# Kernel optimization log

Hardware: AMD Instinct MI355X
Metric: run time of the kernel (lower is better)

Reference implementation:

```python
import jax, jax.numpy as jnp
import numpy as np
import math

B, S, D, H, DH, DFF = 2, 2048, 2048, 16, 128, 8192
EPS = 1e-6
K_AMB = -1.0


def log_map_origin(x, K):
    # x: (..., d+1) Lorentz point -> tangent vector (..., d)
    xi = x[..., 1:]
    n = jnp.sqrt(jnp.sum(xi * xi, axis=-1, keepdims=True))
    a = jnp.sqrt(-K) * n
    # asinh(a)/a, stable near 0 (on-manifold, acosh(sqrt(-K)x0) == asinh(sqrt(-K)||xi||))
    f = jnp.where(a < 1e-6, 1.0 - a * a / 6.0, jnp.arcsinh(a) / jnp.maximum(a, 1e-12))
    return f * xi


def exp_map_stable(v, K):
    # v: (..., d) tangent -> Lorentz point (..., d+1); x0 from exact constraint
    n = jnp.sqrt(jnp.sum(v * v, axis=-1, keepdims=True))
    a = jnp.sqrt(-K) * n
    sinc = jnp.where(a < 1e-6, 1.0 + a * a / 6.0, jnp.sinh(a) / jnp.maximum(a, 1e-12))
    xi = sinc * v
    x0 = jnp.sqrt(-1.0 / K + jnp.sum(xi * xi, axis=-1, keepdims=True))
    return jnp.concatenate([x0, xi], axis=-1)


def lorentz_rmsnorm(x, scale):
    v = log_map_origin(x, K_AMB)
    rms = jnp.sqrt(jnp.mean(v * v, axis=-1, keepdims=True) + EPS)
    return exp_map_stable(scale * (v / rms), K_AMB)


def per_head_attention(x_normed, mask, Wq, Wk, Wv, Wo, head_K):
    v = log_map_origin(x_normed, K_AMB)  # (B,S,D)
    def split(w):
        return (v @ w).reshape(B, S, H, DH).transpose(0, 2, 1, 3)  # (B,H,S,DH)
    q, k, vv = split(Wq), split(Wk), split(Wv)
    Kh = head_K[None, :, None, None]  # (1,H,1,1) per-head curvature
    ql = exp_map_stable(q, Kh)  # (B,H,S,DH+1)
    kl = exp_map_stable(k, Kh)
    # Lorentz inner product <q,k>_L = -q0 k0 + qi.ki via signed metric
    metric = jnp.concatenate([-jnp.ones((1,)), jnp.ones((DH,))])
    L = jnp.einsum('bhqd,bhkd->bhqk', ql * metric, kl)
    # negative squared-distance proxy: 2<q,k>_L - 2/K  (zero when q==k)
    scores = (2.0 * L - 2.0 / Kh) / math.sqrt(DH)
    scores = jnp.where(mask[None, None, :, :], scores, -1e30)
    attn = jax.nn.softmax(scores, axis=-1)
    out = jnp.einsum('bhqk,bhkd->bhqd', attn, vv)  # (B,H,S,DH)
    out = out.transpose(0, 2, 1, 3).reshape(B, S, H * DH)
    return out @ Wo  # Euclidean (B,S,D)


def block_forward(x, mask, scale1, scale2, Wq, Wk, Wv, Wo, head_K, W1, W2):
    xn = lorentz_rmsnorm(x, scale1)
    attn_out = per_head_attention(xn, mask, Wq, Wk, Wv, Wo, head_K)
    x = exp_map_stable(log_map_origin(x, K_AMB) + attn_out, K_AMB)
    xn = lorentz_rmsnorm(x, scale2)
    vf = log_map_origin(xn, K_AMB)
    ffn_eu_pre = jax.nn.gelu(vf @ W1, approximate=False) @ W2
    ffn_out = exp_map_stable(ffn_eu_pre, K_AMB)
    x = exp_map_stable(log_map_origin(x, K_AMB) + log_map_origin(ffn_out, K_AMB), K_AMB)
    return x


def setup_inputs() -> dict:
    key = jax.random.key(0)
    ks = jax.random.split(key, 9)
    v0 = jax.random.normal(ks[0], (B, S, D), jnp.float32) * 0.02
    x = exp_map_stable(v0, K_AMB)  # on-manifold input (B,S,D+1)
    mask = jnp.tril(jnp.ones((S, S), bool))  # causal: True = attend
    init_scale = 1.0 / math.sqrt(D)
    w_std = 0.02
    return {
        'x': x,
        'mask': mask,
        'scale1': jnp.full((D,), init_scale, jnp.float32),
        'scale2': jnp.full((D,), init_scale, jnp.float32),
        'Wq': jax.random.normal(ks[1], (D, H * DH), jnp.float32) * w_std,
        'Wk': jax.random.normal(ks[2], (D, H * DH), jnp.float32) * w_std,
        'Wv': jax.random.normal(ks[3], (D, H * DH), jnp.float32) * w_std,
        'Wo': jax.random.normal(ks[4], (H * DH, D), jnp.float32) * w_std,
        'head_K': jnp.full((H,), -1.0, jnp.float32),
        'W1': jax.random.normal(ks[5], (D, DFF), jnp.float32) * w_std,
        'W2': jax.random.normal(ks[6], (DFF, D), jnp.float32) * w_std,
    }


def reference(x, mask, scale1, scale2, Wq, Wk, Wv, Wo, head_K, W1, W2):
    return block_forward(x, mask, scale1, scale2, Wq, Wk, Wv, Wo, head_K, W1, W2)
```

## Files before the change

kernel.cpp:

```cpp
#include <hip/hip_runtime.h>
#include <stdint.h>

typedef unsigned short u16;
typedef __attribute__((ext_vector_type(8))) short bf16x8;
typedef __attribute__((ext_vector_type(4))) float f32x4;

#define SEQ    2048
#define NB     2
#define NHEAD  16
#define DHEAD  128
#define DMODEL 2048
#define DFFN   8192
#define MROWS  4096

__device__ __forceinline__ u16 f2bf(float x) {
  union { float f; uint32_t u; } v; v.f = x;
  return (u16)((v.u + 0x7fffu + ((v.u >> 16) & 1u)) >> 16);
}
__device__ __forceinline__ float bf2f(u16 h) {
  union { uint32_t u; float f; } v; v.u = ((uint32_t)h) << 16;
  return v.f;
}
__device__ __forceinline__ void gload16(const void* g, void* l) {
  __builtin_amdgcn_global_load_lds((const __attribute__((address_space(1))) void*)g,
                                   (__attribute__((address_space(3))) void*)l,
                                   16, 0, 0);
}
__device__ __forceinline__ float blockSum256(float v) {
  __shared__ float red[4];
  #pragma unroll
  for (int m = 1; m < 64; m <<= 1) v += __shfl_xor(v, m, 64);
  int w = threadIdx.x >> 6;
  if ((threadIdx.x & 63) == 0) red[w] = v;
  __syncthreads();
  float s = red[0] + red[1] + red[2] + red[3];
  __syncthreads();
  return s;
}

__global__ void transpose_w(const float* __restrict__ in, u16* __restrict__ out, int R, int C) {
  __shared__ float tile[32][33];
  int c0 = blockIdx.x * 32, r0 = blockIdx.y * 32;
  int tx = threadIdx.x, ty = threadIdx.y;
  #pragma unroll
  for (int i = 0; i < 4; ++i)
    tile[ty + 8*i][tx] = in[(size_t)(r0 + ty + 8*i) * C + c0 + tx];
  __syncthreads();
  #pragma unroll
  for (int i = 0; i < 4; ++i)
    out[(size_t)(c0 + ty + 8*i) * R + r0 + tx] = f2bf(tile[tx][ty + 8*i]);
}

__global__ void ln_first(const float* __restrict__ x, const float* __restrict__ scale,
                         float* __restrict__ v1, u16* __restrict__ t1) {
  int row = blockIdx.x;
  const float* xr = x + (size_t)row * (DMODEL + 1) + 1;
  float vals[8]; float ss = 0.f;
  #pragma unroll
  for (int i = 0; i < 8; ++i) {
    int idx = threadIdx.x + 256 * i;
    vals[i] = xr[idx];
    ss += vals[i] * vals[i];
  }
  ss = blockSum256(ss);
  float n = sqrtf(ss);
  float f = (n < 1e-6f) ? (1.0f - n * n * (1.0f/6.0f)) : (asinhf(n) / n);
  float rms = sqrtf(f * f * ss * (1.0f / DMODEL) + 1e-6f);
  float ir = 1.0f / rms;
  #pragma unroll
  for (int i = 0; i < 8; ++i) {
    int idx = threadIdx.x + 256 * i;
    float v = f * vals[i];
    v1[(size_t)row * DMODEL + idx] = v;
    t1[(size_t)row * DMODEL + idx] = f2bf(scale[idx] * v * ir);
  }
}

__global__ void rms_mid(const float* __restrict__ u, const float* __restrict__ scale,
                        u16* __restrict__ t) {
  int row = blockIdx.x;
  const float* ur = u + (size_t)row * DMODEL;
  float vals[8]; float ss = 0.f;
  #pragma unroll
  for (int i = 0; i < 8; ++i) { int idx = threadIdx.x + 256*i; vals[i] = ur[idx]; ss += vals[i]*vals[i]; }
  ss = blockSum256(ss);
  float ir = 1.0f / sqrtf(ss * (1.0f / DMODEL) + 1e-6f);
  #pragma unroll
  for (int i = 0; i < 8; ++i) {
    int idx = threadIdx.x + 256*i;
    t[(size_t)row*DMODEL + idx] = f2bf(scale[idx]*vals[i]*ir);
  }
}

__global__ void final_exp(const float* __restrict__ u, float* __restrict__ out) {
  int row = blockIdx.x;
  const float* ur = u + (size_t)row * DMODEL;
  float vals[8]; float ss = 0.f;
  #pragma unroll
  for (int i = 0; i < 8; ++i) { int idx = threadIdx.x + 256*i; vals[i] = ur[idx]; ss += vals[i]*vals[i]; }
  ss = blockSum256(ss);
  float n = sqrtf(ss);
  float f = (n < 1e-6f) ? (1.0f + n*n*(1.0f/6.0f)) : (sinhf(n)/n);
  float* orow = out + (size_t)row * (DMODEL + 1);
  if (threadIdx.x == 0) orow[0] = sqrtf(1.0f + f*f*ss);
  #pragma unroll
  for (int i = 0; i < 8; ++i) { int idx = threadIdx.x + 256*i; orow[1+idx] = f*vals[i]; }
}

template<int EPI>
__global__ __launch_bounds__(256, 3) void gemm_bt(
    const u16* __restrict__ A, const u16* __restrict__ Bt,
    u16* __restrict__ Cb, float* Cf, const float* add,
    int M, int N, int K)
{
  __shared__ u16 As[128 * 32];
  __shared__ u16 Bs[128 * 32];
  const int tid = threadIdx.x;
  const int w = tid >> 6, lane = tid & 63;
  const int lrow = lane & 15, kq = lane >> 4;
  const int m0 = blockIdx.y * 128, n0 = blockIdx.x * 128;
  const int wm = w >> 1, wn = w & 1;
  f32x4 acc[4][4] = {};
  for (int k0 = 0; k0 < K; k0 += 32) {
    __syncthreads();
    #pragma unroll
    for (int j = 0; j < 2; ++j) {
      int ebase = j * 2048 + w * 512;
      int e = ebase + lane * 8;
      int row = e >> 5, col = e & 31;
      gload16(A  + (size_t)(m0 + row) * K + k0 + col, &As[ebase]);
      gload16(Bt + (size_t)(n0 + row) * K + k0 + col, &Bs[ebase]);
    }
    __syncthreads();
    bf16x8 av[4], bv[4];
    #pragma unroll
    for (int i = 0; i < 4; ++i) av[i] = *(const bf16x8*)&As[(wm*64 + i*16 + lrow)*32 + kq*8];
    #pragma unroll
    for (int j = 0; j < 4; ++j) bv[j] = *(const bf16x8*)&Bs[(wn*64 + j*16 + lrow)*32 + kq*8];
    #pragma unroll
    for (int i = 0; i < 4; ++i)
      #pragma unroll
      for (int j = 0; j < 4; ++j)
        acc[i][j] = __builtin_amdgcn_mfma_f32_16x16x32_bf16(av[i], bv[j], acc[i][j], 0, 0, 0);
  }
  #pragma unroll
  for (int i = 0; i < 4; ++i)
    #pragma unroll
    for (int j = 0; j < 4; ++j)
      #pragma unroll
      for (int r = 0; r < 4; ++r) {
        int row = m0 + wm*64 + i*16 + kq*4 + r;
        int col = n0 + wn*64 + j*16 + lrow;
        size_t idx = (size_t)row * N + col;
        float v = acc[i][j][r];
        if (EPI == 0) {
          Cb[idx] = f2bf(v);
        } else if (EPI == 1) {
          Cf[idx] = v + add[idx];
        } else {
          float g = 0.5f * v * (1.0f + erff(v * 0.70710678118654752f));
          Cb[idx] = f2bf(g);
        }
      }
}

__global__ void prep_qk(const u16* __restrict__ in, const float* __restrict__ headK,
                        u16* __restrict__ Lout, float* __restrict__ l0,
                        int instride, int off) {
  int gid = blockIdx.x * 4 + (threadIdx.x >> 6);
  int lane = threadIdx.x & 63;
  int b = gid >> 15;
  int rem = gid & 32767;
  int h = rem >> 11;
  int s = rem & 2047;
  const u16* src = in + ((size_t)(b * SEQ + s)) * instride + off + h * DHEAD + lane * 2;
  float v0 = bf2f(src[0]), v1 = bf2f(src[1]);
  float nn = v0*v0 + v1*v1;
  #pragma unroll
  for (int m = 1; m < 64; m <<= 1) nn += __shfl_xor(nn, m, 64);
  float Kh = headK[h];
  float sk = sqrtf(-Kh);
  float a = sk * sqrtf(nn);
  float f = (a < 1e-6f) ? (1.0f + a*a*(1.0f/6.0f)) : (sinhf(a) / a);
  u16* dst = Lout + (size_t)gid * DHEAD + lane * 2;
  dst[0] = f2bf(f * v0);
  dst[1] = f2bf(f * v1);
  if (lane == 0) l0[gid] = sqrtf(-1.0f/Kh + f*f*nn);
}

__global__ void vtrans(const u16* __restrict__ vb, u16* __restrict__ VT,
                       int instride, int off) {
  __shared__ u16 tile[32][33];
  int bh = blockIdx.x;
  int b = bh >> 4, h = bh & 15;
  int s0 = blockIdx.y * 32, d0 = blockIdx.z * 32;
  int tx = threadIdx.x, ty = threadIdx.y;
  #pragma unroll
  for (int i = 0; i < 4; ++i)
    tile[ty + 8*i][tx] = vb[((size_t)(b*SEQ + s0 + ty + 8*i)) * instride + off + h*DHEAD + d0 + tx];
  __syncthreads();
  #pragma unroll
  for (int i = 0; i < 4; ++i)
    VT[((size_t)bh*DHEAD + d0 + ty + 8*i) * SEQ + s0 + tx] = tile[tx][ty + 8*i];
}

__global__ __launch_bounds__(256, 2) void attn_kernel(
    const u16* __restrict__ Ql, const u16* __restrict__ Kl,
    const u16* __restrict__ VT, const float* __restrict__ ql0,
    const float* __restrict__ kl0, const float* __restrict__ headK,
    u16* __restrict__ out) {
  __shared__ u16 klds[2][32 * 128];
  __shared__ u16 vlds[2][128 * 32];
  __shared__ u16 plds[4][32 * 36];
  const int tid = threadIdx.x, w = tid >> 6, lane = tid & 63;
  const int lrow = lane & 15, kq = lane >> 4;
  const int id = blockIdx.x;
  const int bh = id & 31;
  const int qb = 15 - (id >> 5);
  const int q0 = qb * 128 + w * 32;
  const int b = bh >> 4, h = bh & 15;
  const float Kh = headK[h];
  const float LOG2E = 1.44269504088896f;
  const float isd = 0.088388347648318447f;
  const float sc_mul = 2.0f * isd * LOG2E;
  const float sc_add = (-2.0f / Kh) * isd * LOG2E;

  const u16* kbase  = Kl + (size_t)bh * SEQ * DHEAD;
  const u16* vtbase = VT + (size_t)bh * DHEAD * SEQ;
  const float* kl0b = kl0 + (size_t)bh * SEQ;
  u16* pw = &plds[w][0];

  bf16x8 aq[2][4];
  const u16* qbase = Ql + ((size_t)bh * SEQ + q0) * DHEAD;
  #pragma unroll
  for (int m = 0; m < 2; ++m)
    #pragma unroll
    for (int dc = 0; dc < 4; ++dc)
      aq[m][dc] = *(const bf16x8*)&qbase[(size_t)(m*16 + lrow) * DHEAD + dc*32 + kq*8];
  float q0r[2][4];
  #pragma unroll
  for (int m = 0; m < 2; ++m)
    #pragma unroll
    for (int r = 0; r < 4; ++r)
      q0r[m][r] = ql0[(size_t)bh * SEQ + q0 + m*16 + kq*4 + r];

  auto stage = [&](int k0, int buf) {
    #pragma unroll
    for (int i = 0; i < 2; ++i) {
      int rl = w*8 + i*4 + (lane >> 4);
      int c = (lane & 15) ^ (rl & 15);
      gload16(kbase + ((size_t)(k0 + rl)) * DHEAD + c * 8,
              &klds[buf][(w*8 + i*4) * 128]);
    }
    #pragma unroll
    for (int i = 0; i < 2; ++i) {
      int rl = w*32 + i*16 + (lane >> 2);
      int c = (lane & 3) ^ ((rl >> 1) & 3);
      gload16(vtbase + (size_t)rl * SEQ + k0 + c * 8,
              &vlds[buf][(w*32 + i*16) * 32]);
    }
  };

  float lacc[2][4] = {};
  f32x4 o[2][8] = {};
  const int niter = qb * 4 + 4;

  stage(0, 0);
  for (int i = 0; i < niter; ++i) {
    const int k0 = i * 32, buf = i & 1;
    float kc0 = kl0b[k0 + lrow];
    float kc1 = kl0b[k0 + 16 + lrow];
    if (i + 1 < niter) {
      stage(k0 + 32, buf ^ 1);
      asm volatile("s_waitcnt vmcnt(4)" ::: "memory");
    } else {
      asm volatile("s_waitcnt vmcnt(0)" ::: "memory");
    }
    asm volatile("s_barrier" ::: "memory");

    f32x4 sc[2][2] = {};
    #pragma unroll
    for (int dc = 0; dc < 4; ++dc) {
      int c = dc*4 + kq;
      bf16x8 bk0 = *(const bf16x8*)&klds[buf][lrow*128        + (c ^ (lrow & 15)) * 8];
      bf16x8 bk1 = *(const bf16x8*)&klds[buf][(16 + lrow)*128 + (c ^ ((16 + lrow) & 15)) * 8];
      #pragma unroll
      for (int m = 0; m < 2; ++m) {
        sc[m][0] = __builtin_amdgcn_mfma_f32_16x16x32_bf16(aq[m][dc], bk0, sc[m][0], 0, 0, 0);
        sc[m][1] = __builtin_amdgcn_mfma_f32_16x16x32_bf16(aq[m][dc], bk1, sc[m][1], 0, 0, 0);
      }
    }
    #pragma unroll
    for (int m = 0; m < 2; ++m)
      #pragma unroll
      for (int r = 0; r < 4; ++r) {
        int qg = q0 + m*16 + kq*4 + r;
        float p0 = exp2f((sc[m][0][r] - q0r[m][r] * kc0) * sc_mul + sc_add);
        float p1 = exp2f((sc[m][1][r] - q0r[m][r] * kc1) * sc_mul + sc_add);
        p0 = (k0 + lrow      <= qg) ? p0 : 0.f;
        p1 = (k0 + 16 + lrow <= qg) ? p1 : 0.f;
        lacc[m][r] += p0 + p1;
        pw[(m*16 + kq*4 + r) * 36 + lrow]      = f2bf(p0);
        pw[(m*16 + kq*4 + r) * 36 + 16 + lrow] = f2bf(p1);
      }
    bf16x8 ap0 = *(const bf16x8*)&pw[(size_t)lrow * 36 + kq*8];
    bf16x8 ap1 = *(const bf16x8*)&pw[(size_t)(16 + lrow) * 36 + kq*8];
    int vc = (kq ^ ((lrow >> 1) & 3)) * 8;
    #pragma unroll
    for (int n = 0; n < 8; ++n) {
      bf16x8 bv = *(const bf16x8*)&vlds[buf][(n*16 + lrow) * 32 + vc];
      o[0][n] = __builtin_amdgcn_mfma_f32_16x16x32_bf16(ap0, bv, o[0][n], 0, 0, 0);
      o[1][n] = __builtin_amdgcn_mfma_f32_16x16x32_bf16(ap1, bv, o[1][n], 0, 0, 0);
    }
    asm volatile("s_barrier" ::: "memory");
  }

  float rcl[2][4];
  #pragma unroll
  for (int m = 0; m < 2; ++m)
    #pragma unroll
    for (int r = 0; r < 4; ++r) {
      float s = lacc[m][r];
      #pragma unroll
      for (int mm = 1; mm < 16; mm <<= 1) s += __shfl_xor(s, mm, 16);
      rcl[m][r] = 1.0f / s;
    }
  #pragma unroll
  for (int m = 0; m < 2; ++m)
    #pragma unroll
    for (int n = 0; n < 8; ++n)
      #pragma unroll
      for (int r = 0; r < 4; ++r) {
        int qg = q0 + m*16 + kq*4 + r;
        out[((size_t)b * SEQ + qg) * DMODEL + h * DHEAD + n*16 + lrow] =
            f2bf(o[m][n][r] * rcl[m][r]);
      }
}

extern "C" void kernel_launch(void* const* d_in, const int* in_sizes, int n_in,
                              void* d_out, int out_size, void* d_ws, size_t ws_size,
                              hipStream_t stream) {
  const float* x      = (const float*)d_in[0];
  const float* scale1 = (const float*)d_in[2];
  const float* scale2 = (const float*)d_in[3];
  const float* Wq     = (const float*)d_in[4];
  const float* Wk     = (const float*)d_in[5];
  const float* Wv     = (const float*)d_in[6];
  const float* Wo     = (const float*)d_in[7];
  const float* headK  = (const float*)d_in[8];
  const float* W1     = (const float*)d_in[9];
  const float* W2     = (const float*)d_in[10];
  float* out = (float*)d_out;

  char* p = (char*)d_ws;
  size_t off = 0;
  auto take = [&](size_t bytes) -> char* {
    char* r = p + off;
    off += (bytes + 255) & ~(size_t)255;
    return r;
  };
  u16* WqT = (u16*)take((size_t)DMODEL*DMODEL*2);
  u16* WkT = (u16*)take((size_t)DMODEL*DMODEL*2);
  u16* WvT = (u16*)take((size_t)DMODEL*DMODEL*2);
  u16* WoT = (u16*)take((size_t)DMODEL*DMODEL*2);
  u16* W1T = (u16*)take((size_t)DMODEL*DFFN*2);
  u16* W2T = (u16*)take((size_t)DMODEL*DFFN*2);
  float* vres = (float*)take((size_t)MROWS*DMODEL*4);
  u16* tbuf = (u16*)take((size_t)MROWS*DMODEL*2);
  u16* qkvb = (u16*)take((size_t)MROWS*3*DMODEL*2);
  u16* Qlb  = (u16*)take((size_t)MROWS*DMODEL*2);
  u16* Klb  = (u16*)take((size_t)MROWS*DMODEL*2);
  u16* VTb  = (u16*)take((size_t)MROWS*DMODEL*2);
  float* q0b = (float*)take((size_t)NB*NHEAD*SEQ*4);
  float* k0b = (float*)take((size_t)NB*NHEAD*SEQ*4);
  u16* hbuf = qkvb;
  u16* attnout = tbuf;

  dim3 tb(32, 8);
  transpose_w<<<dim3(DMODEL/32, DMODEL/32), tb, 0, stream>>>(Wq, WqT, DMODEL, DMODEL);
  transpose_w<<<dim3(DMODEL/32, DMODEL/32), tb, 0, stream>>>(Wk, WkT, DMODEL, DMODEL);
  transpose_w<<<dim3(DMODEL/32, DMODEL/32), tb, 0, stream>>>(Wv, WvT, DMODEL, DMODEL);
  transpose_w<<<dim3(DMODEL/32, DMODEL/32), tb, 0, stream>>>(Wo, WoT, DMODEL, DMODEL);
  transpose_w<<<dim3(DFFN/32,   DMODEL/32), tb, 0, stream>>>(W1, W1T, DMODEL, DFFN);
  transpose_w<<<dim3(DMODEL/32, DFFN/32),   tb, 0, stream>>>(W2, W2T, DFFN, DMODEL);

  ln_first<<<MROWS, 256, 0, stream>>>(x, scale1, vres, tbuf);

  gemm_bt<0><<<dim3(3*DMODEL/128, MROWS/128), 256, 0, stream>>>(tbuf, WqT, qkvb, nullptr, nullptr, MROWS, 3*DMODEL, DMODEL);

  prep_qk<<<NB*NHEAD*SEQ/4, 256, 0, stream>>>(qkvb, headK, Qlb, q0b, 3*DMODEL, 0);
  prep_qk<<<NB*NHEAD*SEQ/4, 256, 0, stream>>>(qkvb, headK, Klb, k0b, 3*DMODEL, DMODEL);
  vtrans<<<dim3(NB*NHEAD, SEQ/32, DHEAD/32), tb, 0, stream>>>(qkvb, VTb, 3*DMODEL, 2*DMODEL);

  attn_kernel<<<dim3(512), 256, 0, stream>>>(Qlb, Klb, VTb, q0b, k0b, headK, attnout);

  gemm_bt<1><<<dim3(DMODEL/128, MROWS/128), 256, 0, stream>>>(attnout, WoT, nullptr, vres, vres, MROWS, DMODEL, DMODEL);

  rms_mid<<<MROWS, 256, 0, stream>>>(vres, scale2, tbuf);

  gemm_bt<2><<<dim3(DFFN/128, MROWS/128), 256, 0, stream>>>(tbuf, W1T, hbuf, nullptr, nullptr, MROWS, DFFN, DMODEL);

  gemm_bt<1><<<dim3(DMODEL/128, MROWS/128), 256, 0, stream>>>(hbuf, W2T, nullptr, vres, vres, MROWS, DMODEL, DFFN);

  final_exp<<<MROWS, 256, 0, stream>>>(vres, out);

  (void)in_sizes; (void)n_in; (void)out_size; (void)ws_size;
}
```

Before: 1.015 ms.

## Replace GEMM with 256x256 tiled, double-buffered, swizzled-LDS 512-thread kernel

Replaces the 128x128 single-buffered GEMM with a 256x256 tile kernel using 8 waves, 64-wide K steps, and double-buffered LDS with prefetch of the next tiles interleaved between MFMA phases. It adds an XOR swizzle on LDS addresses to avoid bank conflicts, s_setprio around MFMA bursts, and a block-ID remap for L2 locality across XCDs. The aim is to hide global-load latency and raise MFMA utilization in all four GEMMs. In exchange it uses 128KB of LDS per block and hand-placed waitcnt/barriers, which is fragile, and the grid for the N=2048 GEMMs is small at 128 blocks.

```diff
diff --git a/kernel.cpp b/kernel.cpp
--- a/kernel.cpp
+++ b/kernel.cpp
@@ -108,48 +108,147 @@
 }
 
 template<int EPI>
-__global__ __launch_bounds__(256, 3) void gemm_bt(
+__global__ __launch_bounds__(512, 2) void gemm256(
     const u16* __restrict__ A, const u16* __restrict__ Bt,
     u16* __restrict__ Cb, float* Cf, const float* add,
     int M, int N, int K)
 {
-  __shared__ u16 As[128 * 32];
-  __shared__ u16 Bs[128 * 32];
+  __shared__ __attribute__((aligned(128))) char smem[131072];
   const int tid = threadIdx.x;
   const int w = tid >> 6, lane = tid & 63;
   const int lrow = lane & 15, kq = lane >> 4;
-  const int m0 = blockIdx.y * 128, n0 = blockIdx.x * 128;
-  const int wm = w >> 1, wn = w & 1;
-  f32x4 acc[4][4] = {};
-  for (int k0 = 0; k0 < K; k0 += 32) {
-    __syncthreads();
-    #pragma unroll
-    for (int j = 0; j < 2; ++j) {
-      int ebase = j * 2048 + w * 512;
-      int e = ebase + lane * 8;
-      int row = e >> 5, col = e & 31;
-      gload16(A  + (size_t)(m0 + row) * K + k0 + col, &As[ebase]);
-      gload16(Bt + (size_t)(n0 + row) * K + k0 + col, &Bs[ebase]);
-    }
-    __syncthreads();
-    bf16x8 av[4], bv[4];
-    #pragma unroll
-    for (int i = 0; i < 4; ++i) av[i] = *(const bf16x8*)&As[(wm*64 + i*16 + lrow)*32 + kq*8];
-    #pragma unroll
-    for (int j = 0; j < 4; ++j) bv[j] = *(const bf16x8*)&Bs[(wn*64 + j*16 + lrow)*32 + kq*8];
+  const int wm = w >> 2, wn = w & 3;
+
+  const int nwg = gridDim.x;
+  const int cpx = nwg >> 3;
+  const int sid = (blockIdx.x & 7) * cpx + (blockIdx.x >> 3);
+  const int NX = N >> 8;
+  const int bx = sid % NX, by = sid / NX;
+  const int m0 = by * 256, n0 = bx * 256;
+  const int NT = K >> 6;
+
+  size_t goff[2];
+  #pragma unroll
+  for (int r = 0; r < 2; ++r) {
+    int L = r * 8192 + tid * 16;
+    int U = L ^ (((L >> 9) & 1) << 5);
+    int si = U >> 10;
+    int row = (si >> 1) * 16 + ((U >> 6) & 15);
+    int col = (si & 1) * 32 + ((U & 63) >> 1);
+    goff[r] = (size_t)row * K + col;
+  }
+  auto stage_half = [&](const u16* g, int ldsOff) {
+    #pragma unroll
+    for (int r = 0; r < 2; ++r)
+      gload16(g + goff[r], smem + ldsOff + r * 8192 + w * 1024);
+  };
+
+  const u16* A0 = A  + (size_t)m0 * K;
+  const u16* A1 = A  + (size_t)(m0 + 128) * K;
+  const u16* B0 = Bt + (size_t)n0 * K;
+  const u16* B1 = Bt + (size_t)(n0 + 128) * K;
+
+  const int aoff = (lrow * 64 + kq * 16) ^ ((lrow & 8) << 2);
+
+  f32x4 acc[8][4] = {};
+
+  stage_half(A0, 0);
+  stage_half(A1, 16384);
+  stage_half(B0, 32768);
+  stage_half(B1, 49152);
+  stage_half(A0 + 64, 65536);
+  stage_half(A1 + 64, 65536 + 16384);
+  asm volatile("s_waitcnt vmcnt(4)" ::: "memory");
+  asm volatile("s_barrier" ::: "memory");
+
+  for (int t = 0; t < NT; ++t) {
+    const int buf = t & 1;
+    const char* ab = smem + buf * 65536 + wm * 16384 + aoff;
+    const char* bb = smem + buf * 65536 + 32768 + (wn >> 1) * 16384 + (wn & 1) * 8192 + aoff;
+    bf16x8 a0[4][2], a1[4][2], b0[2][2], b1[2][2];
+
     #pragma unroll
     for (int i = 0; i < 4; ++i)
       #pragma unroll
-      for (int j = 0; j < 4; ++j)
-        acc[i][j] = __builtin_amdgcn_mfma_f32_16x16x32_bf16(av[i], bv[j], acc[i][j], 0, 0, 0);
+      for (int kk = 0; kk < 2; ++kk)
+        a0[i][kk] = *(const bf16x8*)(ab + (i*2 + kk) * 1024);
+    #pragma unroll
+    for (int j = 0; j < 2; ++j)
+      #pragma unroll
+      for (int kk = 0; kk < 2; ++kk)
+        b0[j][kk] = *(const bf16x8*)(bb + (j*2 + kk) * 1024);
+    if (t + 1 < NT) stage_half(B0 + (t+1)*64, (buf^1)*65536 + 32768);
+    asm volatile("s_barrier" ::: "memory");
+    __builtin_amdgcn_s_setprio(1);
+    #pragma unroll
+    for (int kk = 0; kk < 2; ++kk)
+      #pragma unroll
+      for (int i = 0; i < 4; ++i)
+        #pragma unroll
+        for (int j = 0; j < 2; ++j)
+          acc[i][j] = __builtin_amdgcn_mfma_f32_16x16x32_bf16(a0[i][kk], b0[j][kk], acc[i][j], 0, 0, 0);
+    __builtin_amdgcn_s_setprio(0);
+    asm volatile("s_barrier" ::: "memory");
+
+    #pragma unroll
+    for (int i = 0; i < 4; ++i)
+      #pragma unroll
+      for (int kk = 0; kk < 2; ++kk)
+        a1[i][kk] = *(const bf16x8*)(ab + ((4 + i)*2 + kk) * 1024);
+    if (t + 1 < NT) stage_half(B1 + (t+1)*64, (buf^1)*65536 + 49152);
+    asm volatile("s_barrier" ::: "memory");
+    __builtin_amdgcn_s_setprio(1);
+    #pragma unroll
+    for (int kk = 0; kk < 2; ++kk)
+      #pragma unroll
+      for (int i = 0; i < 4; ++i)
+        #pragma unroll
+        for (int j = 0; j < 2; ++j)
+          acc[4 + i][j] = __builtin_amdgcn_mfma_f32_16x16x32_bf16(a1[i][kk], b0[j][kk], acc[4 + i][j], 0, 0, 0);
+    __builtin_amdgcn_s_setprio(0);
+    asm volatile("s_barrier" ::: "memory");
+
+    #pragma unroll
+    for (int j = 0; j < 2; ++j)
+      #pragma unroll
+      for (int kk = 0; kk < 2; ++kk)
+        b1[j][kk] = *(const bf16x8*)(bb + ((2 + j)*2 + kk) * 1024);
+    if (t + 2 < NT) stage_half(A0 + (t+2)*64, buf*65536);
+    asm volatile("s_barrier" ::: "memory");
+    __builtin_amdgcn_s_setprio(1);
+    #pragma unroll
+    for (int kk = 0; kk < 2; ++kk)
+      #pragma unroll
+      for (int i = 0; i < 4; ++i)
+        #pragma unroll
+        for (int j = 0; j < 2; ++j)
+          acc[4 + i][2 + j] = __builtin_amdgcn_mfma_f32_16x16x32_bf16(a1[i][kk], b1[j][kk], acc[4 + i][2 + j], 0, 0, 0);
+    __builtin_amdgcn_s_setprio(0);
+    asm volatile("s_barrier" ::: "memory");
+
+    if (t + 2 < NT) stage_half(A1 + (t+2)*64, buf*65536 + 16384);
+    asm volatile("s_barrier" ::: "memory");
+    __builtin_amdgcn_s_setprio(1);
+    #pragma unroll
+    for (int kk = 0; kk < 2; ++kk)
+      #pragma unroll
+      for (int i = 0; i < 4; ++i)
+        #pragma unroll
+        for (int j = 0; j < 2; ++j)
+          acc[i][2 + j] = __builtin_amdgcn_mfma_f32_16x16x32_bf16(a0[i][kk], b1[j][kk], acc[i][2 + j], 0, 0, 0);
+    __builtin_amdgcn_s_setprio(0);
+    if (t + 2 < NT) asm volatile("s_waitcnt vmcnt(4)" ::: "memory");
+    else            asm volatile("s_waitcnt vmcnt(0)" ::: "memory");
+    asm volatile("s_barrier" ::: "memory");
   }
-  #pragma unroll
-  for (int i = 0; i < 4; ++i)
+
+  #pragma unroll
+  for (int i = 0; i < 8; ++i)
     #pragma unroll
     for (int j = 0; j < 4; ++j)
       #pragma unroll
       for (int r = 0; r < 4; ++r) {
-        int row = m0 + wm*64 + i*16 + kq*4 + r;
+        int row = m0 + wm*128 + i*16 + kq*4 + r;
         int col = n0 + wn*64 + j*16 + lrow;
         size_t idx = (size_t)row * N + col;
         float v = acc[i][j][r];
@@ -386,7 +485,8 @@
 
   ln_first<<<MROWS, 256, 0, stream>>>(x, scale1, vres, tbuf);
 
-  gemm_bt<0><<<dim3(3*DMODEL/128, MROWS/128), 256, 0, stream>>>(tbuf, WqT, qkvb, nullptr, nullptr, MROWS, 3*DMODEL, DMODEL);
+  gemm256<0><<<dim3((3*DMODEL/256)*(MROWS/256)), 512, 0, stream>>>(
+      tbuf, WqT, qkvb, nullptr, nullptr, MROWS, 3*DMODEL, DMODEL);
 
   prep_qk<<<NB*NHEAD*SEQ/4, 256, 0, stream>>>(qkvb, headK, Qlb, q0b, 3*DMODEL, 0);
   prep_qk<<<NB*NHEAD*SEQ/4, 256, 0, stream>>>(qkvb, headK, Klb, k0b, 3*DMODEL, DMODEL);
@@ -394,13 +494,16 @@
 
   attn_kernel<<<dim3(512), 256, 0, stream>>>(Qlb, Klb, VTb, q0b, k0b, headK, attnout);
 
-  gemm_bt<1><<<dim3(DMODEL/128, MROWS/128), 256, 0, stream>>>(attnout, WoT, nullptr, vres, vres, MROWS, DMODEL, DMODEL);
+  gemm256<1><<<dim3((DMODEL/256)*(MROWS/256)), 512, 0, stream>>>(
+      attnout, WoT, nullptr, vres, vres, MROWS, DMODEL, DMODEL);
 
   rms_mid<<<MROWS, 256, 0, stream>>>(vres, scale2, tbuf);
 
-  gemm_bt<2><<<dim3(DFFN/128, MROWS/128), 256, 0, stream>>>(tbuf, W1T, hbuf, nullptr, nullptr, MROWS, DFFN, DMODEL);
-
-  gemm_bt<1><<<dim3(DMODEL/128, MROWS/128), 256, 0, stream>>>(hbuf, W2T, nullptr, vres, vres, MROWS, DMODEL, DFFN);
+  gemm256<2><<<dim3((DFFN/256)*(MROWS/256)), 512, 0, stream>>>(
+      tbuf, W1T, hbuf, nullptr, nullptr, MROWS, DFFN, DMODEL);
+
+  gemm256<1><<<dim3((DMODEL/256)*(MROWS/256)), 512, 0, stream>>>(
+      hbuf, W2T, nullptr, vres, vres, MROWS, DMODEL, DFFN);
 
   final_exp<<<MROWS, 256, 0, stream>>>(vres, out);
 
```

After: 1.003 ms. No clear change (-1.2%).
